# Kernel optimization log

Hardware: AMD Instinct MI355X
Metric: run time of the kernel (lower is better)

Reference implementation:

```python
import jax, jax.numpy as jnp
import numpy as np

N = 50000
E = 600000
IN = 128
HID = 128
OUT = 64
EPS = 1e-5


def layernorm(x, g, b):
    mu = jnp.mean(x, axis=-1, keepdims=True)
    var = jnp.mean(jnp.square(x - mu), axis=-1, keepdims=True)
    return (x - mu) * jax.lax.rsqrt(var + EPS) * g + b


def film_layer(x, W, Fm, g, b, src, dst):
    # x: [N, d_in]; W: [d_out, d_in]; Fm: [2*d_out, d_in]
    m = x @ W.T                       # [N, d_out]
    fw = x @ Fm.T                     # [N, 2*d_out]
    d_out = W.shape[0]
    gamma, beta = fw[:, :d_out], fw[:, d_out:]
    msg = jax.nn.relu(gamma * m + beta)           # [N, d_out]
    h = jax.ops.segment_sum(msg[src], dst, num_segments=N)  # scatter-sum over edges
    return layernorm(h, g, b)  # dropout is identity in eval mode


def setup_inputs() -> dict:
    key = jax.random.key(0)
    ks = jax.random.split(key, 12)
    s = lambda fan_in: 1.0 / np.sqrt(fan_in)
    return {
        "features": jax.random.normal(ks[0], (N, IN), dtype=jnp.float32),
        "src": jax.random.randint(ks[1], (E,), 0, N, dtype=jnp.int32),
        "dst": jax.random.randint(ks[2], (E,), 0, N, dtype=jnp.int32),
        "W1": jax.random.uniform(ks[3], (HID, IN), jnp.float32, -s(IN), s(IN)),
        "F1": jax.random.uniform(ks[4], (2 * HID, IN), jnp.float32, -s(IN), s(IN)),
        "g1": jnp.ones((HID,), jnp.float32),
        "b1": jnp.zeros((HID,), jnp.float32),
        "W2": jax.random.uniform(ks[5], (HID, HID), jnp.float32, -s(HID), s(HID)),
        "F2": jax.random.uniform(ks[6], (2 * HID, HID), jnp.float32, -s(HID), s(HID)),
        "g2": jnp.ones((HID,), jnp.float32),
        "b2": jnp.zeros((HID,), jnp.float32),
        "Wp": jax.random.uniform(ks[7], (OUT, HID), jnp.float32, -s(HID), s(HID)),
        "bp": jax.random.uniform(ks[8], (OUT,), jnp.float32, -s(HID), s(HID)),
    }


def reference(features, src, dst, W1, F1, g1, b1, W2, F2, g2, b2, Wp, bp):
    h = film_layer(features, W1, F1, g1, b1, src, dst)
    h = film_layer(h, W2, F2, g2, b2, src, dst)
    return jax.nn.sigmoid(h @ Wp.T + bp)  # [N, OUT]
```

## Files before the change

kernel.cpp:

```cpp
#include <hip/hip_runtime.h>
#include <hip/hip_bf16.h>
#include <math.h>

#define IN_D 128
#define HID_D 128
#define OUT_D 64
#define CAP 64

typedef __attribute__((ext_vector_type(8))) short bf16x8;
typedef __attribute__((ext_vector_type(4))) float f32x4;

__device__ __forceinline__ unsigned short f2bf(float f) {
    unsigned u = __float_as_uint(f);
    u += 0x7fffu + ((u >> 16) & 1u);
    return (unsigned short)(u >> 16);
}
__device__ __forceinline__ float bf2f(unsigned short h) {
    return __uint_as_float(((unsigned)h) << 16);
}

__global__ __launch_bounds__(256) void k_fill_prep(
        const int* __restrict__ src_idx, const int* __restrict__ dst_idx,
        int* __restrict__ cnt, unsigned short* __restrict__ elist, int E,
        const float* __restrict__ W1, const float* __restrict__ F1,
        const float* __restrict__ W2, const float* __restrict__ F2,
        const float* __restrict__ Wp,
        unsigned short* __restrict__ wc1, unsigned short* __restrict__ wc2,
        unsigned short* __restrict__ wpb) {
    int e = blockIdx.x * 256 + threadIdx.x;
    if (e < E) {
        int d = dst_idx[e];
        int pos = atomicAdd(&cnt[d], 1);
        elist[(size_t)d * CAP + pos] = (unsigned short)src_idx[e];
    }
    const int NW = HID_D * IN_D;
    const int NC = 3 * NW;
    const int NP = OUT_D * HID_D;
    int i = e;
    if (i < NC) {
        wc1[i] = f2bf(i < NW ? W1[i] : F1[i - NW]);
    } else if (i < 2 * NC) {
        int j = i - NC;
        wc2[j] = f2bf(j < NW ? W2[j] : F2[j - NW]);
    } else if (i < 2 * NC + NP) {
        int j = i - 2 * NC;
        wpb[j] = f2bf(Wp[j]);
    }
}

__device__ __forceinline__ bf16x8 load_frag(const unsigned short* p) {
    return *(const bf16x8*)p;
}
__device__ __forceinline__ bf16x8 load_frag(const float* p) {
    float4 u = ((const float4*)p)[0];
    float4 w = ((const float4*)p)[1];
    bf16x8 r;
    r[0] = (short)f2bf(u.x); r[1] = (short)f2bf(u.y);
    r[2] = (short)f2bf(u.z); r[3] = (short)f2bf(u.w);
    r[4] = (short)f2bf(w.x); r[5] = (short)f2bf(w.y);
    r[6] = (short)f2bf(w.z); r[7] = (short)f2bf(w.w);
    return r;
}

template <typename XT>
__global__ __launch_bounds__(256, 2) void k_msg(const XT* __restrict__ X,
                                                const unsigned short* __restrict__ Wc,
                                                unsigned short* __restrict__ Msg,
                                                int n, int nchunks) {
    const int wave = threadIdx.x >> 6;
    const int lane = threadIdx.x & 63;
    const int lr = lane & 15;
    const int quad = lane >> 4;
    const int t0 = wave * 2;
    const int tidx[6] = {t0, t0 + 1, t0 + 8, t0 + 9, t0 + 16, t0 + 17};

    bf16x8 b[6][4];
    #pragma unroll
    for (int u = 0; u < 6; u++)
        #pragma unroll
        for (int s = 0; s < 4; s++)
            b[u][s] = *(const bf16x8*)(Wc + (size_t)(16 * tidx[u] + lr) * IN_D + quad * 8 + 32 * s);

    for (int c = blockIdx.x; c < nchunks; c += gridDim.x) {
        const int row0 = c << 5;

        bf16x8 a[2][4];
        #pragma unroll
        for (int rt = 0; rt < 2; rt++) {
            int r = row0 + rt * 16 + lr;
            if (r > n - 1) r = n - 1;
            const XT* xp = X + (size_t)r * IN_D + quad * 8;
            #pragma unroll
            for (int s = 0; s < 4; s++) a[rt][s] = load_frag(xp + 32 * s);
        }

        f32x4 acc[6][2];
        #pragma unroll
        for (int u = 0; u < 6; u++)
            #pragma unroll
            for (int rt = 0; rt < 2; rt++) acc[u][rt] = (f32x4){0.f, 0.f, 0.f, 0.f};

        #pragma unroll
        for (int s = 0; s < 4; s++)
            #pragma unroll
            for (int u = 0; u < 6; u++)
                #pragma unroll
                for (int rt = 0; rt < 2; rt++)
                    acc[u][rt] = __builtin_amdgcn_mfma_f32_16x16x32_bf16(a[rt][s], b[u][s], acc[u][rt], 0, 0, 0);

        #pragma unroll
        for (int u = 0; u < 2; u++) {
            #pragma unroll
            for (int rt = 0; rt < 2; rt++) {
                #pragma unroll
                for (int r = 0; r < 4; r++) {
                    int row = row0 + rt * 16 + quad * 4 + r;
                    if (row < n) {
                        float v = acc[2 + u][rt][r] * acc[u][rt][r] + acc[4 + u][rt][r];
                        v = v > 0.f ? v : 0.f;
                        Msg[(size_t)row * HID_D + 16 * (t0 + u) + lr] = f2bf(v);
                    }
                }
            }
        }
    }
}

__global__ __launch_bounds__(256) void k_agg_ln(const unsigned short* __restrict__ Msg,
                                                const unsigned short* __restrict__ elist,
                                                const int* __restrict__ cnt,
                                                const float* __restrict__ gamma,
                                                const float* __restrict__ beta,
                                                unsigned short* __restrict__ Hout, int n) {
    int node = blockIdx.x * 4 + (threadIdx.x >> 6);
    int lane = threadIdx.x & 63;
    int half = lane >> 5;
    int l = lane & 31;
    if (node >= n) return;
    const unsigned short* seg = elist + (size_t)node * CAP;
    int deg = cnt[node];
    int myidx = seg[lane];
    float a0 = 0.f, a1 = 0.f, a2 = 0.f, a3 = 0.f;

#define ACC4(v) { a0 += bf2f((unsigned short)((v).x & 0xffffu)); \
                  a1 += bf2f((unsigned short)((v).x >> 16));     \
                  a2 += bf2f((unsigned short)((v).y & 0xffffu)); \
                  a3 += bf2f((unsigned short)((v).y >> 16)); }

    int i = 0;
    for (; i + 4 <= deg; i += 4) {
        int iA = __shfl(myidx, i + half);
        int iB = __shfl(myidx, i + 2 + half);
        uint2 vA = *(const uint2*)(Msg + (size_t)iA * HID_D + l * 4);
        uint2 vB = *(const uint2*)(Msg + (size_t)iB * HID_D + l * 4);
        ACC4(vA);
        ACC4(vB);
    }
    for (; i + 2 <= deg; i += 2) {
        int iA = __shfl(myidx, i + half);
        uint2 vA = *(const uint2*)(Msg + (size_t)iA * HID_D + l * 4);
        ACC4(vA);
    }
    if (i < deg && half == 0) {
        int iA = __shfl(myidx, i);
        uint2 vA = *(const uint2*)(Msg + (size_t)iA * HID_D + l * 4);
        ACC4(vA);
    }
#undef ACC4

    a0 += __shfl_xor(a0, 32);
    a1 += __shfl_xor(a1, 32);
    a2 += __shfl_xor(a2, 32);
    a3 += __shfl_xor(a3, 32);

    float s = a0 + a1 + a2 + a3;
    float sq = a0 * a0 + a1 * a1 + a2 * a2 + a3 * a3;
    #pragma unroll
    for (int d = 16; d; d >>= 1) {
        s += __shfl_xor(s, d);
        sq += __shfl_xor(sq, d);
    }
    float mu = s * (1.f / 128.f);
    float var = sq * (1.f / 128.f) - mu * mu;
    float rs = rsqrtf(var + 1e-5f);
    float4 g4 = ((const float4*)gamma)[l];
    float4 b4 = ((const float4*)beta)[l];
    float y0 = (a0 - mu) * rs * g4.x + b4.x;
    float y1 = (a1 - mu) * rs * g4.y + b4.y;
    float y2 = (a2 - mu) * rs * g4.z + b4.z;
    float y3 = (a3 - mu) * rs * g4.w + b4.w;
    if (half == 0) {
        uint2 o;
        o.x = (unsigned)f2bf(y0) | ((unsigned)f2bf(y1) << 16);
        o.y = (unsigned)f2bf(y2) | ((unsigned)f2bf(y3) << 16);
        *(uint2*)(Hout + (size_t)node * HID_D + l * 4) = o;
    }
}

__global__ __launch_bounds__(256) void k_proj(const unsigned short* __restrict__ H,
                                              const unsigned short* __restrict__ Wpb,
                                              const float* __restrict__ bp,
                                              float* __restrict__ out, int n) {
    const int row0 = blockIdx.x << 6;
    const int wave = threadIdx.x >> 6;
    const int lane = threadIdx.x & 63;
    const int lr = lane & 15;
    const int quad = lane >> 4;

    f32x4 acc[4];
    #pragma unroll
    for (int rt = 0; rt < 4; rt++) acc[rt] = (f32x4){0.f, 0.f, 0.f, 0.f};

    #pragma unroll
    for (int s = 0; s < 4; s++) {
        bf16x8 bv = *(const bf16x8*)(Wpb + (size_t)(16 * wave + lr) * HID_D + quad * 8 + 32 * s);
        #pragma unroll
        for (int rt = 0; rt < 4; rt++) {
            int r = row0 + rt * 16 + lr;
            if (r > n - 1) r = n - 1;
            bf16x8 av = *(const bf16x8*)(H + (size_t)r * HID_D + quad * 8 + 32 * s);
            acc[rt] = __builtin_amdgcn_mfma_f32_16x16x32_bf16(av, bv, acc[rt], 0, 0, 0);
        }
    }
    float bias = bp[16 * wave + lr];
    #pragma unroll
    for (int rt = 0; rt < 4; rt++) {
        #pragma unroll
        for (int r = 0; r < 4; r++) {
            int row = row0 + rt * 16 + quad * 4 + r;
            if (row < n) {
                float z = acc[rt][r] + bias;
                out[(size_t)row * OUT_D + 16 * wave + lr] = 1.f / (1.f + __expf(-z));
            }
        }
    }
}

extern "C" void kernel_launch(void* const* d_in, const int* in_sizes, int n_in,
                              void* d_out, int out_size, void* d_ws, size_t ws_size,
                              hipStream_t stream) {
    const float* features = (const float*)d_in[0];
    const int* src = (const int*)d_in[1];
    const int* dst = (const int*)d_in[2];
    const float* W1 = (const float*)d_in[3];
    const float* F1 = (const float*)d_in[4];
    const float* g1 = (const float*)d_in[5];
    const float* b1 = (const float*)d_in[6];
    const float* W2 = (const float*)d_in[7];
    const float* F2 = (const float*)d_in[8];
    const float* g2 = (const float*)d_in[9];
    const float* b2 = (const float*)d_in[10];
    const float* Wp = (const float*)d_in[11];
    const float* bp = (const float*)d_in[12];

    const int N = in_sizes[0] / IN_D;
    const int E = in_sizes[1];
    float* out = (float*)d_out;

    char* p = (char*)d_ws;
    auto alloc = [&](size_t b) -> char* {
        char* r = p;
        p += (b + 255) & ~(size_t)255;
        return r;
    };
    unsigned short* buf0 = (unsigned short*)alloc((size_t)N * HID_D * 2);
    unsigned short* buf1 = (unsigned short*)alloc((size_t)N * HID_D * 2);
    unsigned short* wc1  = (unsigned short*)alloc((size_t)3 * HID_D * IN_D * 2);
    unsigned short* wc2  = (unsigned short*)alloc((size_t)3 * HID_D * HID_D * 2);
    unsigned short* wpb  = (unsigned short*)alloc((size_t)OUT_D * HID_D * 2);
    int* cnt    = (int*)alloc((size_t)N * 4);
    unsigned short* elist = (unsigned short*)alloc((size_t)N * CAP * 2);

    const int eb = (E + 255) / 256;
    const int mc = (N + 31) / 32;
    const int mg = 512;
    const int pb = (N + 63) / 64;
    const int ab = (N + 3) / 4;

    hipMemsetAsync(cnt, 0, (size_t)N * 4, stream);
    k_fill_prep<<<eb, 256, 0, stream>>>(src, dst, cnt, elist, E,
                                        W1, F1, W2, F2, Wp, wc1, wc2, wpb);

    k_msg<float><<<mg, 256, 0, stream>>>(features, wc1, buf1, N, mc);
    k_agg_ln<<<ab, 256, 0, stream>>>(buf1, elist, cnt, g1, b1, buf0, N);
    k_msg<unsigned short><<<mg, 256, 0, stream>>>(buf0, wc2, buf1, N, mc);
    k_agg_ln<<<ab, 256, 0, stream>>>(buf1, elist, cnt, g2, b2, buf0, N);
    k_proj<<<pb, 256, 0, stream>>>(buf0, wpb, bp, out, N);
}
```

Baseline: 234.5 us.

## Pre-convert features to bf16 in prep kernel and halve k_msg row tile

The fp32-to-bf16 conversion of the input features moves into the existing edge-fill/weight-prep kernel, writing a bf16 copy to workspace so the first message GEMM reads bf16 directly like the second layer. k_msg is de-templated, and each chunk now covers 16 rows instead of 32, so there are twice as many chunks and fewer accumulator registers. This cuts conversion work and register pressure in the GEMM. In exchange it adds an extra write and read of the bf16 feature copy, and it gives less weight-fragment reuse per chunk.

```diff
diff --git a/kernel.cpp b/kernel.cpp
--- a/kernel.cpp
+++ b/kernel.cpp
@@ -25,6 +25,7 @@
         const float* __restrict__ W1, const float* __restrict__ F1,
         const float* __restrict__ W2, const float* __restrict__ F2,
         const float* __restrict__ Wp,
+        const float* __restrict__ X, unsigned short* __restrict__ fx, int nfv,
         unsigned short* __restrict__ wc1, unsigned short* __restrict__ wc2,
         unsigned short* __restrict__ wpb) {
     int e = blockIdx.x * 256 + threadIdx.x;
@@ -32,6 +33,21 @@
         int d = dst_idx[e];
         int pos = atomicAdd(&cnt[d], 1);
         elist[(size_t)d * CAP + pos] = (unsigned short)src_idx[e];
+    }
+    if (e < nfv) {
+        const float4* xp = (const float4*)X + (size_t)e * 4;
+        float4 v0 = xp[0], v1 = xp[1], v2 = xp[2], v3 = xp[3];
+        uint4 o0, o1;
+        o0.x = (unsigned)f2bf(v0.x) | ((unsigned)f2bf(v0.y) << 16);
+        o0.y = (unsigned)f2bf(v0.z) | ((unsigned)f2bf(v0.w) << 16);
+        o0.z = (unsigned)f2bf(v1.x) | ((unsigned)f2bf(v1.y) << 16);
+        o0.w = (unsigned)f2bf(v1.z) | ((unsigned)f2bf(v1.w) << 16);
+        o1.x = (unsigned)f2bf(v2.x) | ((unsigned)f2bf(v2.y) << 16);
+        o1.y = (unsigned)f2bf(v2.z) | ((unsigned)f2bf(v2.w) << 16);
+        o1.z = (unsigned)f2bf(v3.x) | ((unsigned)f2bf(v3.y) << 16);
+        o1.w = (unsigned)f2bf(v3.z) | ((unsigned)f2bf(v3.w) << 16);
+        ((uint4*)fx)[(size_t)e * 2]     = o0;
+        ((uint4*)fx)[(size_t)e * 2 + 1] = o1;
     }
     const int NW = HID_D * IN_D;
     const int NC = 3 * NW;
@@ -48,22 +64,7 @@
     }
 }
 
-__device__ __forceinline__ bf16x8 load_frag(const unsigned short* p) {
-    return *(const bf16x8*)p;
-}
-__device__ __forceinline__ bf16x8 load_frag(const float* p) {
-    float4 u = ((const float4*)p)[0];
-    float4 w = ((const float4*)p)[1];
-    bf16x8 r;
-    r[0] = (short)f2bf(u.x); r[1] = (short)f2bf(u.y);
-    r[2] = (short)f2bf(u.z); r[3] = (short)f2bf(u.w);
-    r[4] = (short)f2bf(w.x); r[5] = (short)f2bf(w.y);
-    r[6] = (short)f2bf(w.z); r[7] = (short)f2bf(w.w);
-    return r;
-}
-
-template <typename XT>
-__global__ __launch_bounds__(256, 2) void k_msg(const XT* __restrict__ X,
+__global__ __launch_bounds__(256, 2) void k_msg(const unsigned short* __restrict__ X,
                                                 const unsigned short* __restrict__ Wc,
                                                 unsigned short* __restrict__ Msg,
                                                 int n, int nchunks) {
@@ -82,44 +83,34 @@
             b[u][s] = *(const bf16x8*)(Wc + (size_t)(16 * tidx[u] + lr) * IN_D + quad * 8 + 32 * s);
 
     for (int c = blockIdx.x; c < nchunks; c += gridDim.x) {
-        const int row0 = c << 5;
-
-        bf16x8 a[2][4];
-        #pragma unroll
-        for (int rt = 0; rt < 2; rt++) {
-            int r = row0 + rt * 16 + lr;
-            if (r > n - 1) r = n - 1;
-            const XT* xp = X + (size_t)r * IN_D + quad * 8;
-            #pragma unroll
-            for (int s = 0; s < 4; s++) a[rt][s] = load_frag(xp + 32 * s);
-        }
-
-        f32x4 acc[6][2];
-        #pragma unroll
-        for (int u = 0; u < 6; u++)
-            #pragma unroll
-            for (int rt = 0; rt < 2; rt++) acc[u][rt] = (f32x4){0.f, 0.f, 0.f, 0.f};
+        const int row0 = c << 4;
+
+        int r = row0 + lr;
+        if (r > n - 1) r = n - 1;
+        const unsigned short* xp = X + (size_t)r * IN_D + quad * 8;
+        bf16x8 a[4];
+        #pragma unroll
+        for (int s = 0; s < 4; s++) a[s] = *(const bf16x8*)(xp + 32 * s);
+
+        f32x4 acc[6];
+        #pragma unroll
+        for (int u = 0; u < 6; u++) acc[u] = (f32x4){0.f, 0.f, 0.f, 0.f};
 
         #pragma unroll
         for (int s = 0; s < 4; s++)
             #pragma unroll
             for (int u = 0; u < 6; u++)
-                #pragma unroll
-                for (int rt = 0; rt < 2; rt++)
-                    acc[u][rt] = __builtin_amdgcn_mfma_f32_16x16x32_bf16(a[rt][s], b[u][s], acc[u][rt], 0, 0, 0);
+                acc[u] = __builtin_amdgcn_mfma_f32_16x16x32_bf16(a[s], b[u][s], acc[u], 0, 0, 0);
 
         #pragma unroll
         for (int u = 0; u < 2; u++) {
             #pragma unroll
-            for (int rt = 0; rt < 2; rt++) {
-                #pragma unroll
-                for (int r = 0; r < 4; r++) {
-                    int row = row0 + rt * 16 + quad * 4 + r;
-                    if (row < n) {
-                        float v = acc[2 + u][rt][r] * acc[u][rt][r] + acc[4 + u][rt][r];
-                        v = v > 0.f ? v : 0.f;
-                        Msg[(size_t)row * HID_D + 16 * (t0 + u) + lr] = f2bf(v);
-                    }
+            for (int rr = 0; rr < 4; rr++) {
+                int row = row0 + quad * 4 + rr;
+                if (row < n) {
+                    float v = acc[2 + u][rr] * acc[u][rr] + acc[4 + u][rr];
+                    v = v > 0.f ? v : 0.f;
+                    Msg[(size_t)row * HID_D + 16 * (t0 + u) + lr] = f2bf(v);
                 }
             }
         }
@@ -265,6 +256,7 @@
     };
     unsigned short* buf0 = (unsigned short*)alloc((size_t)N * HID_D * 2);
     unsigned short* buf1 = (unsigned short*)alloc((size_t)N * HID_D * 2);
+    unsigned short* fx   = (unsigned short*)alloc((size_t)N * IN_D * 2);
     unsigned short* wc1  = (unsigned short*)alloc((size_t)3 * HID_D * IN_D * 2);
     unsigned short* wc2  = (unsigned short*)alloc((size_t)3 * HID_D * HID_D * 2);
     unsigned short* wpb  = (unsigned short*)alloc((size_t)OUT_D * HID_D * 2);
@@ -272,18 +264,20 @@
     unsigned short* elist = (unsigned short*)alloc((size_t)N * CAP * 2);
 
     const int eb = (E + 255) / 256;
-    const int mc = (N + 31) / 32;
+    const int mc = (N + 15) / 16;
     const int mg = 512;
     const int pb = (N + 63) / 64;
     const int ab = (N + 3) / 4;
+    const int nfv = (N * IN_D) / 16;
 
     hipMemsetAsync(cnt, 0, (size_t)N * 4, stream);
     k_fill_prep<<<eb, 256, 0, stream>>>(src, dst, cnt, elist, E,
-                                        W1, F1, W2, F2, Wp, wc1, wc2, wpb);
-
-    k_msg<float><<<mg, 256, 0, stream>>>(features, wc1, buf1, N, mc);
+                                        W1, F1, W2, F2, Wp,
+                                        features, fx, nfv, wc1, wc2, wpb);
+
+    k_msg<<<mg, 256, 0, stream>>>(fx, wc1, buf1, N, mc);
     k_agg_ln<<<ab, 256, 0, stream>>>(buf1, elist, cnt, g1, b1, buf0, N);
-    k_msg<unsigned short><<<mg, 256, 0, stream>>>(buf0, wc2, buf1, N, mc);
+    k_msg<<<mg, 256, 0, stream>>>(buf0, wc2, buf1, N, mc);
     k_agg_ln<<<ab, 256, 0, stream>>>(buf1, elist, cnt, g2, b2, buf0, N);
     k_proj<<<pb, 256, 0, stream>>>(buf0, wpb, bp, out, N);
 }
```

Result: no change. 233.5 us (-0.4%).
